# Optimization experiments

Measured on AMD Instinct MI355X. Metric: run time of the kernel, lower is better.

## Reference

```python
import jax, jax.numpy as jnp
import numpy as np

N_NODES = 50000
N_EDGES = 1600000
IN_FEATS = 512
N_HIDDEN = 128
N_CLASSES = 40


def setup_inputs() -> dict:
    key = jax.random.key(0)
    k1, k2, k3, k4, k5, k6, k7 = jax.random.split(key, 7)
    features = jax.random.normal(k1, (N_NODES, IN_FEATS), dtype=jnp.float32)
    src = jax.random.randint(k2, (N_EDGES,), 0, N_NODES)
    dst = jax.random.randint(k3, (N_EDGES,), 0, N_NODES)
    # Glorot-ish init for weights, zeros for biases (DGL GraphConv defaults)
    W1 = jax.random.normal(k4, (IN_FEATS, N_HIDDEN), dtype=jnp.float32) / np.sqrt(IN_FEATS)
    b1 = jnp.zeros((N_HIDDEN,), dtype=jnp.float32)
    W2 = jax.random.normal(k5, (N_HIDDEN, N_CLASSES), dtype=jnp.float32) / np.sqrt(N_HIDDEN)
    b2 = jnp.zeros((N_CLASSES,), dtype=jnp.float32)
    return {"features": features, "W1": W1, "b1": b1, "W2": W2, "b2": b2,
            "src": src, "dst": dst}


def _norms(src, dst, n_nodes):
    ones = jnp.ones(src.shape[0], dtype=jnp.float32)
    deg_out = jax.ops.segment_sum(ones, src, num_segments=n_nodes)
    deg_in = jax.ops.segment_sum(ones, dst, num_segments=n_nodes)
    # clamp degree >= 1 as DGL does
    norm_src = jax.lax.rsqrt(jnp.maximum(deg_out, 1.0))
    norm_dst = jax.lax.rsqrt(jnp.maximum(deg_in, 1.0))
    return norm_src, norm_dst


def _graph_conv(x, W, b, src, dst, norm_src, norm_dst, n_nodes):
    # DGL GraphConv with norm='both'; in_feats > out_feats so W applied first
    h = x @ W                                   # [N, out]
    h = h * norm_src[:, None]                   # src-side D^{-1/2}
    msgs = h[src]                               # gather [E, out]
    agg = jax.ops.segment_sum(msgs, dst, num_segments=n_nodes)  # scatter-add
    agg = agg * norm_dst[:, None]               # dst-side D^{-1/2}
    return agg + b


def reference(features, W1, b1, W2, b2, src, dst):
    norm_src, norm_dst = _norms(src, dst, N_NODES)
    h = _graph_conv(features, W1, b1, src, dst, norm_src, norm_dst, N_NODES)
    h = jax.nn.relu(h)
    # dropout is identity at inference
    h = _graph_conv(h, W2, b2, src, dst, norm_src, norm_dst, N_NODES)
    return h
```

## Files before the change

### kernel.cpp

```cpp
#include <hip/hip_runtime.h>
#include <hip/hip_bf16.h>

#define N_NODES 50000
#define N_EDGES 1600000
#define IN_FEATS 512
#define N_HIDDEN 128
#define N_CLASSES 40
#define NBKT 782
#define NBLK 800
#define EPB 2000
#define NROWPAD 50048

typedef __attribute__((ext_vector_type(8))) short bf16x8;
typedef __attribute__((ext_vector_type(4))) float f32x4;

__device__ __forceinline__ unsigned short f2bf(float f) {
    unsigned u = __float_as_uint(f);
    u = (u + 0x7FFFu + ((u >> 16) & 1u)) >> 16;
    return (unsigned short)u;
}
__device__ __forceinline__ float bf2f(unsigned short h) {
    return __uint_as_float(((unsigned)h) << 16);
}
__device__ __forceinline__ unsigned pk_bf(float a, float b) {
    __hip_bfloat162 h = __float22bfloat162_rn(make_float2(a, b));
    union { __hip_bfloat162 v; unsigned u; } c;
    c.v = h;
    return c.u;
}

__global__ __launch_bounds__(256) void setup_cvt(
    const float* __restrict__ W1, const float* __restrict__ W2,
    unsigned short* __restrict__ W1ch, unsigned short* __restrict__ W1cl,
    unsigned short* __restrict__ W2th, unsigned short* __restrict__ W2tl) {
    int i = blockIdx.x * 256 + threadIdx.x;
    if (i < IN_FEATS * N_HIDDEN) {
        int k = i >> 7, c = i & 127;
        float v = W1[i];
        unsigned short h = f2bf(v);
        int o = (k >> 5) * 4096 + c * 32 + (k & 31);
        W1ch[o] = h;
        W1cl[o] = f2bf(v - bf2f(h));
    } else {
        int j = i - IN_FEATS * N_HIDDEN;
        int n = j >> 7, k = j & 127;
        float v = (n < N_CLASSES) ? W2[k * N_CLASSES + n] : 0.f;
        unsigned short h = f2bf(v);
        W2th[n * 128 + k] = h;
        W2tl[n * 128 + k] = f2bf(v - bf2f(h));
    }
}

__global__ __launch_bounds__(256) void megaA(
    const int* __restrict__ src, const int* __restrict__ dst,
    int* __restrict__ histD, int* __restrict__ histS,
    const float* __restrict__ X, const unsigned short* __restrict__ Wch,
    const unsigned short* __restrict__ Wcl, unsigned short* __restrict__ Hb) {
    __shared__ int hd[NBKT], hs[NBKT];
    __shared__ __align__(16) unsigned short Xh[64][40];
    __shared__ __align__(16) unsigned short Xl[64][40];
    const int tid = threadIdx.x;

    if (blockIdx.x < NBLK) {
        int b = blockIdx.x;
        for (int i = tid; i < NBKT; i += 256) { hd[i] = 0; hs[i] = 0; }
        __syncthreads();
        int e0 = b * EPB;
        for (int i = tid; i < EPB; i += 256) {
            atomicAdd(&hd[dst[e0 + i] >> 6], 1);
            atomicAdd(&hs[src[e0 + i] >> 6], 1);
        }
        __syncthreads();
        for (int i = tid; i < NBKT; i += 256) {
            histD[b * NBKT + i] = hd[i];
            histS[b * NBKT + i] = hs[i];
        }
        return;
    }
    const int lane = tid & 63;
    const int wv = tid >> 6;
    const int m = lane & 15;
    const int q = lane >> 4;
    const int row0 = (blockIdx.x - NBLK) * 64;

    const int r0 = tid >> 3,          kq0 = (tid & 7) * 4;
    const int r1 = (tid + 256) >> 3,  kq1 = (tid & 7) * 4;
    const bool g0 = (row0 + r0) < N_NODES;
    const bool g1 = (row0 + r1) < N_NODES;
    const float* xp0 = &X[(size_t)(row0 + r0) * IN_FEATS + kq0];
    const float* xp1 = &X[(size_t)(row0 + r1) * IN_FEATS + kq1];

    f32x4 acc[4][2];
#pragma unroll
    for (int i = 0; i < 4; i++)
#pragma unroll
        for (int j = 0; j < 2; j++) acc[i][j] = (f32x4){0.f, 0.f, 0.f, 0.f};

    float4 xa0 = g0 ? *(const float4*)xp0 : make_float4(0.f, 0.f, 0.f, 0.f);
    float4 xa1 = g1 ? *(const float4*)xp1 : make_float4(0.f, 0.f, 0.f, 0.f);

    for (int kc = 0; kc < 16; kc++) {
        {
            unsigned h0 = pk_bf(xa0.x, xa0.y), h1 = pk_bf(xa0.z, xa0.w);
            unsigned l0 = pk_bf(xa0.x - __uint_as_float(h0 << 16),
                                xa0.y - __uint_as_float(h0 & 0xffff0000u));
            unsigned l1 = pk_bf(xa0.z - __uint_as_float(h1 << 16),
                                xa0.w - __uint_as_float(h1 & 0xffff0000u));
            *(uint2*)&Xh[r0][kq0] = make_uint2(h0, h1);
            *(uint2*)&Xl[r0][kq0] = make_uint2(l0, l1);
            unsigned h2 = pk_bf(xa1.x, xa1.y), h3 = pk_bf(xa1.z, xa1.w);
            unsigned l2 = pk_bf(xa1.x - __uint_as_float(h2 << 16),
                                xa1.y - __uint_as_float(h2 & 0xffff0000u));
            unsigned l3 = pk_bf(xa1.z - __uint_as_float(h3 << 16),
                                xa1.w - __uint_as_float(h3 & 0xffff0000u));
            *(uint2*)&Xh[r1][kq1] = make_uint2(h2, h3);
            *(uint2*)&Xl[r1][kq1] = make_uint2(l2, l3);
        }
        __syncthreads();
        if (kc < 15) {
            xa0 = g0 ? *(const float4*)(xp0 + (kc + 1) * 32) : make_float4(0.f, 0.f, 0.f, 0.f);
            xa1 = g1 ? *(const float4*)(xp1 + (kc + 1) * 32) : make_float4(0.f, 0.f, 0.f, 0.f);
        }
        bf16x8 bh[2], bl[2];
#pragma unroll
        for (int j = 0; j < 2; j++) {
            int o = kc * 4096 + (wv * 32 + j * 16 + m) * 32 + q * 8;
            bh[j] = *(const bf16x8*)&Wch[o];
            bl[j] = *(const bf16x8*)&Wcl[o];
        }
        bf16x8 ah[4], al[4];
#pragma unroll
        for (int i = 0; i < 4; i++) {
            ah[i] = *(const bf16x8*)&Xh[i * 16 + m][q * 8];
            al[i] = *(const bf16x8*)&Xl[i * 16 + m][q * 8];
        }
#pragma unroll
        for (int i = 0; i < 4; i++)
#pragma unroll
            for (int j = 0; j < 2; j++) {
                acc[i][j] = __builtin_amdgcn_mfma_f32_16x16x32_bf16(ah[i], bh[j], acc[i][j], 0, 0, 0);
                acc[i][j] = __builtin_amdgcn_mfma_f32_16x16x32_bf16(ah[i], bl[j], acc[i][j], 0, 0, 0);
                acc[i][j] = __builtin_amdgcn_mfma_f32_16x16x32_bf16(al[i], bh[j], acc[i][j], 0, 0, 0);
            }
        __syncthreads();
    }
#pragma unroll
    for (int i = 0; i < 4; i++) {
#pragma unroll
        for (int r = 0; r < 4; r++) {
            int grow = row0 + i * 16 + q * 4 + r;
            if (grow < N_NODES) {
#pragma unroll
                for (int j = 0; j < 2; j++)
                    Hb[(size_t)grow * N_HIDDEN + wv * 32 + j * 16 + m] = f2bf(acc[i][j][r]);
            }
        }
    }
}

__global__ __launch_bounds__(256) void p2_local(
    const int* __restrict__ histD, const int* __restrict__ histS,
    int* __restrict__ baseD, int* __restrict__ baseS,
    int* __restrict__ totD, int* __restrict__ totS) {
    int wv = threadIdx.x >> 6, lane = threadIdx.x & 63;
    int w = blockIdx.x * 4 + wv;
    if (w >= NBKT) return;
    int runD = 0, runS = 0;
#pragma unroll
    for (int c = 0; c < 13; c++) {
        int blk = c * 64 + lane;
        int vD = 0, vS = 0;
        if (blk < NBLK) {
            vD = histD[blk * NBKT + w];
            vS = histS[blk * NBKT + w];
        }
        int iD = vD, iS = vS;
#pragma unroll
        for (int off = 1; off < 64; off <<= 1) {
            int tD = __shfl_up(iD, off);
            int tS = __shfl_up(iS, off);
            if (lane >= off) { iD += tD; iS += tS; }
        }
        if (blk < NBLK) {
            baseD[blk * NBKT + w] = runD + iD - vD;
            baseS[blk * NBKT + w] = runS + iS - vS;
        }
        runD += __shfl(iD, 63);
        runS += __shfl(iS, 63);
    }
    if (lane == 0) { totD[w] = runD; totS[w] = runS; }
}

__global__ __launch_bounds__(1024) void p2_small(
    const int* __restrict__ totD, const int* __restrict__ totS,
    int* __restrict__ bucket_base, int* __restrict__ srcb_base,
    int* __restrict__ offsets) {
    __shared__ int part[1024];
    int t = threadIdx.x;
    int v = (t < NBKT) ? totD[t] : 0;
    part[t] = v;
    __syncthreads();
    for (int off = 1; off < 1024; off <<= 1) {
        int x = (t >= off) ? part[t - off] : 0;
        __syncthreads();
        part[t] += x;
        __syncthreads();
    }
    if (t < NBKT) bucket_base[t] = part[t] - v;
    if (t == 0) { bucket_base[NBKT] = N_EDGES; offsets[N_NODES] = N_EDGES; }
    __syncthreads();
    v = (t < NBKT) ? totS[t] : 0;
    part[t] = v;
    __syncthreads();
    for (int off = 1; off < 1024; off <<= 1) {
        int x = (t >= off) ? part[t - off] : 0;
        __syncthreads();
        part[t] += x;
        __syncthreads();
    }
    if (t < NBKT) srcb_base[t] = part[t] - v;
    if (t == 0) srcb_base[NBKT] = N_EDGES;
}

__global__ __launch_bounds__(256) void p3_scatter(
    const int* __restrict__ src, const int* __restrict__ dst,
    const int* __restrict__ baseD, const int* __restrict__ baseS,
    const int* __restrict__ bucket_base, const int* __restrict__ srcb_base,
    unsigned int* __restrict__ edata, unsigned char* __restrict__ srcv) {
    __shared__ int curD[NBKT], curS[NBKT];
    int t = threadIdx.x, b = blockIdx.x;
    for (int i = t; i < NBKT; i += 256) {
        curD[i] = bucket_base[i] + baseD[b * NBKT + i];
        curS[i] = srcb_base[i] + baseS[b * NBKT + i];
    }
    __syncthreads();
    int e0 = b * EPB;
    for (int i = t; i < EPB; i += 256) {
        int s = src[e0 + i], d = dst[e0 + i];
        int slotD = atomicAdd(&curD[d >> 6], 1);
        edata[slotD] = (unsigned)s | ((unsigned)(d & 63) << 16);
        int slotS = atomicAdd(&curS[s >> 6], 1);
        srcv[slotS] = (unsigned char)(s & 63);
    }
}

__global__ __launch_bounds__(256) void p4_fused(
    const int* __restrict__ srcb_base, const unsigned char* __restrict__ srcv,
    const int* __restrict__ bucket_base, const unsigned int* __restrict__ edata,
    int* __restrict__ offsets, float* __restrict__ norm_src,
    float* __restrict__ norm_dst, int* __restrict__ sorted_src) {
    __shared__ int cntS[64], cntD[64], cur[64];
    int t = threadIdx.x, b = blockIdx.x;
    if (t < 64) { cntS[t] = 0; cntD[t] = 0; }
    __syncthreads();
    int s0 = srcb_base[b], s1 = srcb_base[b + 1];
    for (int i = s0 + t; i < s1; i += 256) atomicAdd(&cntS[srcv[i]], 1);
    int d0 = bucket_base[b], d1 = bucket_base[b + 1];
    for (int i = d0 + t; i < d1; i += 256)
        atomicAdd(&cntD[(edata[i] >> 16) & 63], 1);
    __syncthreads();
    if (t == 0) {
        int run = 0;
        for (int i = 0; i < 64; i++) { cur[i] = run; run += cntD[i]; }
    }
    __syncthreads();
    if (t < 64) {
        int node = b * 64 + t;
        if (node < N_NODES) {
            norm_src[node] = rsqrtf(fmaxf((float)cntS[t], 1.0f));
            offsets[node] = d0 + cur[t];
            norm_dst[node] = rsqrtf(fmaxf((float)cntD[t], 1.0f));
        }
    }
    __syncthreads();
    for (int i = d0 + t; i < d1; i += 256) {
        unsigned e = edata[i];
        int slot = atomicAdd(&cur[(e >> 16) & 63], 1);
        sorted_src[d0 + slot] = (int)(e & 0xFFFFu);
    }
}

#define FMA8(W, NS)                                                   \
    acc0 = fmaf(__uint_as_float((W).x << 16), NS, acc0);              \
    acc1 = fmaf(__uint_as_float((W).x & 0xffff0000u), NS, acc1);      \
    acc2 = fmaf(__uint_as_float((W).y << 16), NS, acc2);              \
    acc3 = fmaf(__uint_as_float((W).y & 0xffff0000u), NS, acc3);      \
    acc4 = fmaf(__uint_as_float((W).z << 16), NS, acc4);              \
    acc5 = fmaf(__uint_as_float((W).z & 0xffff0000u), NS, acc5);      \
    acc6 = fmaf(__uint_as_float((W).w << 16), NS, acc6);              \
    acc7 = fmaf(__uint_as_float((W).w & 0xffff0000u), NS, acc7);

__global__ __launch_bounds__(256) void agg1_kernel(
    const int* __restrict__ offsets, const int* __restrict__ sorted_src,
    const unsigned short* __restrict__ Hb, const float* __restrict__ norm_dst,
    const float* __restrict__ norm_src, const float* __restrict__ b1,
    unsigned short* __restrict__ H1h, unsigned short* __restrict__ H1l) {
    int wid = (blockIdx.x * 256 + threadIdx.x) >> 6;
    int lane = threadIdx.x & 63;
    if (wid >= N_NODES) return;
    int start = offsets[wid], end = offsets[wid + 1];
    int quad = lane >> 4;
    int c8 = (lane & 15) * 8;
    float acc0 = 0.f, acc1 = 0.f, acc2 = 0.f, acc3 = 0.f;
    float acc4 = 0.f, acc5 = 0.f, acc6 = 0.f, acc7 = 0.f;
    int base = start;
    for (; base + 16 <= end; base += 16) {
        int e0 = sorted_src[base + quad];
        int e1 = sorted_src[base + 4 + quad];
        int e2 = sorted_src[base + 8 + quad];
        int e3 = sorted_src[base + 12 + quad];
        float n0 = norm_src[e0], n1 = norm_src[e1];
        float n2 = norm_src[e2], n3 = norm_src[e3];
        uint4 w0 = *(const uint4*)&Hb[(size_t)e0 * N_HIDDEN + c8];
        uint4 w1 = *(const uint4*)&Hb[(size_t)e1 * N_HIDDEN + c8];
        uint4 w2 = *(const uint4*)&Hb[(size_t)e2 * N_HIDDEN + c8];
        uint4 w3 = *(const uint4*)&Hb[(size_t)e3 * N_HIDDEN + c8];
        FMA8(w0, n0);
        FMA8(w1, n1);
        FMA8(w2, n2);
        FMA8(w3, n3);
    }
    for (; base + 4 <= end; base += 4) {
        int e = sorted_src[base + quad];
        float n = norm_src[e];
        uint4 w = *(const uint4*)&Hb[(size_t)e * N_HIDDEN + c8];
        FMA8(w, n);
    }
    int rem = end - base;
    if (quad < rem) {
        int e = sorted_src[base + quad];
        float n = norm_src[e];
        uint4 w = *(const uint4*)&Hb[(size_t)e * N_HIDDEN + c8];
        FMA8(w, n);
    }
    acc0 += __shfl_xor(acc0, 16); acc0 += __shfl_xor(acc0, 32);
    acc1 += __shfl_xor(acc1, 16); acc1 += __shfl_xor(acc1, 32);
    acc2 += __shfl_xor(acc2, 16); acc2 += __shfl_xor(acc2, 32);
    acc3 += __shfl_xor(acc3, 16); acc3 += __shfl_xor(acc3, 32);
    acc4 += __shfl_xor(acc4, 16); acc4 += __shfl_xor(acc4, 32);
    acc5 += __shfl_xor(acc5, 16); acc5 += __shfl_xor(acc5, 32);
    acc6 += __shfl_xor(acc6, 16); acc6 += __shfl_xor(acc6, 32);
    acc7 += __shfl_xor(acc7, 16); acc7 += __shfl_xor(acc7, 32);
    if (quad == 0) {
        float nd = norm_dst[wid];
        float ns = norm_src[wid];
        float4 ba = *(const float4*)&b1[c8];
        float4 bb = *(const float4*)&b1[c8 + 4];
        float o[8];
        o[0] = fmaxf(acc0 * nd + ba.x, 0.f) * ns;
        o[1] = fmaxf(acc1 * nd + ba.y, 0.f) * ns;
        o[2] = fmaxf(acc2 * nd + ba.z, 0.f) * ns;
        o[3] = fmaxf(acc3 * nd + ba.w, 0.f) * ns;
        o[4] = fmaxf(acc4 * nd + bb.x, 0.f) * ns;
        o[5] = fmaxf(acc5 * nd + bb.y, 0.f) * ns;
        o[6] = fmaxf(acc6 * nd + bb.z, 0.f) * ns;
        o[7] = fmaxf(acc7 * nd + bb.w, 0.f) * ns;
        unsigned short hh[8], ll[8];
#pragma unroll
        for (int t = 0; t < 8; t++) {
            hh[t] = f2bf(o[t]);
            ll[t] = f2bf(o[t] - bf2f(hh[t]));
        }
        uint4 ph = make_uint4((unsigned)hh[0] | ((unsigned)hh[1] << 16),
                              (unsigned)hh[2] | ((unsigned)hh[3] << 16),
                              (unsigned)hh[4] | ((unsigned)hh[5] << 16),
                              (unsigned)hh[6] | ((unsigned)hh[7] << 16));
        uint4 pl = make_uint4((unsigned)ll[0] | ((unsigned)ll[1] << 16),
                              (unsigned)ll[2] | ((unsigned)ll[3] << 16),
                              (unsigned)ll[4] | ((unsigned)ll[5] << 16),
                              (unsigned)ll[6] | ((unsigned)ll[7] << 16));
        *(uint4*)&H1h[(size_t)wid * N_HIDDEN + c8] = ph;
        *(uint4*)&H1l[(size_t)wid * N_HIDDEN + c8] = pl;
    }
}

__global__ __launch_bounds__(256) void gemm2_kernel(
    const unsigned short* __restrict__ H1h, const unsigned short* __restrict__ H1l,
    const unsigned short* __restrict__ W2th, const unsigned short* __restrict__ W2tl,
    float* __restrict__ H2p) {
    __shared__ __align__(16) unsigned short Bh[48][136];
    __shared__ __align__(16) unsigned short Bl[48][136];
    const int tid = threadIdx.x;
    for (int i = tid; i < 48 * 16; i += 256) {
        int n = i >> 4, kq = (i & 15) * 8;
        *(uint4*)&Bh[n][kq] = *(const uint4*)&W2th[n * 128 + kq];
        *(uint4*)&Bl[n][kq] = *(const uint4*)&W2tl[n * 128 + kq];
    }
    __syncthreads();
    const int lane = tid & 63;
    const int wave = tid >> 6;
    const int m = lane & 15;
    const int q = lane >> 4;
    const int row0 = blockIdx.x * 128 + wave * 32;

    f32x4 acc[2][3];
#pragma unroll
    for (int i = 0; i < 2; i++)
#pragma unroll
        for (int j = 0; j < 3; j++) acc[i][j] = (f32x4){0.f, 0.f, 0.f, 0.f};

#pragma unroll
    for (int kc = 0; kc < 4; kc++) {
        bf16x8 bh[3], bl[3];
#pragma unroll
        for (int j = 0; j < 3; j++) {
            bh[j] = *(const bf16x8*)&Bh[j * 16 + m][kc * 32 + q * 8];
            bl[j] = *(const bf16x8*)&Bl[j * 16 + m][kc * 32 + q * 8];
        }
#pragma unroll
        for (int i = 0; i < 2; i++) {
            size_t ro = (size_t)(row0 + i * 16 + m) * N_HIDDEN + kc * 32 + q * 8;
            bf16x8 ah = *(const bf16x8*)&H1h[ro];
            bf16x8 al = *(const bf16x8*)&H1l[ro];
#pragma unroll
            for (int j = 0; j < 3; j++) {
                acc[i][j] = __builtin_amdgcn_mfma_f32_16x16x32_bf16(ah, bh[j], acc[i][j], 0, 0, 0);
                acc[i][j] = __builtin_amdgcn_mfma_f32_16x16x32_bf16(ah, bl[j], acc[i][j], 0, 0, 0);
                acc[i][j] = __builtin_amdgcn_mfma_f32_16x16x32_bf16(al, bh[j], acc[i][j], 0, 0, 0);
            }
        }
    }
#pragma unroll
    for (int i = 0; i < 2; i++) {
#pragma unroll
        for (int r = 0; r < 4; r++) {
            int row = row0 + i * 16 + q * 4 + r;
            if (row < N_NODES) {
#pragma unroll
                for (int j = 0; j < 3; j++) {
                    int col = j * 16 + m;
                    if (col < N_CLASSES)
                        H2p[(size_t)row * 64 + col] = acc[i][j][r];
                }
            }
        }
    }
}

__global__ __launch_bounds__(256) void agg2_kernel(
    const int* __restrict__ offsets, const int* __restrict__ sorted_src,
    const float* __restrict__ H2p, const float* __restrict__ norm_dst,
    const float* __restrict__ b2, float* __restrict__ OUT) {
    int wid = (blockIdx.x * 256 + threadIdx.x) >> 6;
    int lane = threadIdx.x & 63;
    if (wid >= N_NODES) return;
    int start = offsets[wid], end = offsets[wid + 1];
    int quad = lane >> 4;
    int c4 = (lane & 15) * 4;
    bool active = c4 < N_CLASSES;
    float4 acc = make_float4(0.f, 0.f, 0.f, 0.f);
    int base = start;
    for (; base + 16 <= end; base += 16) {
        int e0 = sorted_src[base + quad];
        int e1 = sorted_src[base + 4 + quad];
        int e2 = sorted_src[base + 8 + quad];
        int e3 = sorted_src[base + 12 + quad];
        if (active) {
            float4 v0 = *(const float4*)&H2p[(size_t)e0 * 64 + c4];
            float4 v1 = *(const float4*)&H2p[(size_t)e1 * 64 + c4];
            float4 v2 = *(const float4*)&H2p[(size_t)e2 * 64 + c4];
            float4 v3 = *(const float4*)&H2p[(size_t)e3 * 64 + c4];
            acc.x += (v0.x + v1.x) + (v2.x + v3.x);
            acc.y += (v0.y + v1.y) + (v2.y + v3.y);
            acc.z += (v0.z + v1.z) + (v2.z + v3.z);
            acc.w += (v0.w + v1.w) + (v2.w + v3.w);
        }
    }
    for (; base + 4 <= end; base += 4) {
        int e = sorted_src[base + quad];
        if (active) {
            float4 v = *(const float4*)&H2p[(size_t)e * 64 + c4];
            acc.x += v.x; acc.y += v.y; acc.z += v.z; acc.w += v.w;
        }
    }
    int rem = end - base;
    if (quad < rem && active) {
        int e = sorted_src[base + quad];
        float4 v = *(const float4*)&H2p[(size_t)e * 64 + c4];
        acc.x += v.x; acc.y += v.y; acc.z += v.z; acc.w += v.w;
    }
    acc.x += __shfl_xor(acc.x, 16); acc.x += __shfl_xor(acc.x, 32);
    acc.y += __shfl_xor(acc.y, 16); acc.y += __shfl_xor(acc.y, 32);
    acc.z += __shfl_xor(acc.z, 16); acc.z += __shfl_xor(acc.z, 32);
    acc.w += __shfl_xor(acc.w, 16); acc.w += __shfl_xor(acc.w, 32);
    if (lane < 10) {
        float nd = norm_dst[wid];
        float4 b = *(const float4*)&b2[lane * 4];
        acc.x = acc.x * nd + b.x;
        acc.y = acc.y * nd + b.y;
        acc.z = acc.z * nd + b.z;
        acc.w = acc.w * nd + b.w;
        *(float4*)&OUT[(size_t)wid * N_CLASSES + lane * 4] = acc;
    }
}

extern "C" void kernel_launch(void* const* d_in, const int* in_sizes, int n_in,
                              void* d_out, int out_size, void* d_ws, size_t ws_size,
                              hipStream_t stream) {
    const float* X   = (const float*)d_in[0];
    const float* W1  = (const float*)d_in[1];
    const float* b1  = (const float*)d_in[2];
    const float* W2  = (const float*)d_in[3];
    const float* b2  = (const float*)d_in[4];
    const int*   src = (const int*)d_in[5];
    const int*   dst = (const int*)d_in[6];
    float* out = (float*)d_out;

    float* norm_src   = (float*)d_ws;
    float* norm_dst   = norm_src + N_NODES;
    int*   offsets    = (int*)(norm_dst + N_NODES);
    int*   bucket_base = offsets + N_NODES + 16;
    int*   srcb_base  = bucket_base + 800;
    unsigned int* edata = (unsigned int*)(srcb_base + 800);
    unsigned char* srcv = (unsigned char*)(edata + N_EDGES);
    int*   sorted_src = (int*)(edata + N_EDGES) + 400000;
    int*   regionA    = sorted_src + N_EDGES;
    int*   histD      = regionA;
    int*   histS      = regionA + 625600;
    int*   baseD      = regionA + 1251200;
    int*   baseS      = regionA + 1876800;
    int*   totD       = regionA + 2502400;
    int*   totS       = regionA + 2503200;
    float* H2p        = (float*)regionA;
    unsigned short* H1h = (unsigned short*)(regionA + 3200000);
    unsigned short* H1l = H1h + (size_t)NROWPAD * N_HIDDEN;
    unsigned short* W1ch = H1l + (size_t)NROWPAD * N_HIDDEN;
    unsigned short* W1cl = W1ch + IN_FEATS * N_HIDDEN;
    unsigned short* W2th = W1cl + IN_FEATS * N_HIDDEN;
    unsigned short* W2tl = W2th + 48 * 128;
    unsigned short* Hb   = W2tl + 48 * 128;

    setup_cvt<<<(IN_FEATS * N_HIDDEN + 48 * 128) / 256, 256, 0, stream>>>(
        W1, W2, W1ch, W1cl, W2th, W2tl);
    megaA<<<NBLK + NBKT, 256, 0, stream>>>(src, dst, histD, histS, X, W1ch, W1cl, Hb);
    p2_local<<<(NBKT + 3) / 4, 256, 0, stream>>>(histD, histS, baseD, baseS, totD, totS);
    p2_small<<<1, 1024, 0, stream>>>(totD, totS, bucket_base, srcb_base, offsets);
    p3_scatter<<<NBLK, 256, 0, stream>>>(src, dst, baseD, baseS, bucket_base, srcb_base,
                                         edata, srcv);
    p4_fused<<<NBKT, 256, 0, stream>>>(srcb_base, srcv, bucket_base, edata,
                                       offsets, norm_src, norm_dst, sorted_src);
    agg1_kernel<<<(N_NODES + 3) / 4, 256, 0, stream>>>(offsets, sorted_src, Hb, norm_dst,
                                                       norm_src, b1, H1h, H1l);
    gemm2_kernel<<<(N_NODES + 127) / 128, 256, 0, stream>>>(H1h, H1l, W2th, W2tl, H2p);
    agg2_kernel<<<(N_NODES + 3) / 4, 256, 0, stream>>>(offsets, sorted_src, H2p, norm_dst, b2, out);
}
```

Measured before the change: 369.0 us.

## Double-buffer X tiles in megaA GEMM with one barrier per k-step

Double-buffers the LDS X tiles in the first-layer GEMM and fully unrolls the 16 k-steps. Each step converts and stores the next chunk while MFMAs run on the current one, with global loads issued two chunks ahead and a single barrier per step instead of two. Histogram and GEMM shared memory now share one raw buffer, and block order is swapped so GEMM blocks come first. The cost is more registers and a larger code footprint.

```diff
diff --git a/kernel.cpp b/kernel.cpp
--- a/kernel.cpp
+++ b/kernel.cpp
@@ -51,18 +51,71 @@
     }
 }
 
+
+#define MF3(AI, BJ, ACC)                                                         \
+    ACC = __builtin_amdgcn_mfma_f32_16x16x32_bf16(ah##AI, bh0##BJ, ACC, 0, 0, 0); \
+    ACC = __builtin_amdgcn_mfma_f32_16x16x32_bf16(ah##AI, bl0##BJ, ACC, 0, 0, 0); \
+    ACC = __builtin_amdgcn_mfma_f32_16x16x32_bf16(al##AI, bh0##BJ, ACC, 0, 0, 0);
+
+#define CONV_STORE(BUF)                                                     \
+    {                                                                       \
+        unsigned h0 = pk_bf(xa0.x, xa0.y), h1 = pk_bf(xa0.z, xa0.w);        \
+        unsigned l0 = pk_bf(xa0.x - __uint_as_float(h0 << 16),              \
+                            xa0.y - __uint_as_float(h0 & 0xffff0000u));     \
+        unsigned l1 = pk_bf(xa0.z - __uint_as_float(h1 << 16),              \
+                            xa0.w - __uint_as_float(h1 & 0xffff0000u));     \
+        *(uint2*)&Xh[BUF][r0][kq0] = make_uint2(h0, h1);                    \
+        *(uint2*)&Xl[BUF][r0][kq0] = make_uint2(l0, l1);                    \
+        unsigned h2 = pk_bf(xa1.x, xa1.y), h3 = pk_bf(xa1.z, xa1.w);        \
+        unsigned l2 = pk_bf(xa1.x - __uint_as_float(h2 << 16),              \
+                            xa1.y - __uint_as_float(h2 & 0xffff0000u));     \
+        unsigned l3 = pk_bf(xa1.z - __uint_as_float(h3 << 16),              \
+                            xa1.w - __uint_as_float(h3 & 0xffff0000u));     \
+        *(uint2*)&Xh[BUF][r1][kq0] = make_uint2(h2, h3);                    \
+        *(uint2*)&Xl[BUF][r1][kq0] = make_uint2(l2, l3);                    \
+    }
+
+#define STEP(CUR, NXT, KC)                                                  \
+    {                                                                       \
+        bf16x8 bh00 = *(const bf16x8*)(wbh + (KC) * 4096);                  \
+        bf16x8 bh01 = *(const bf16x8*)(wbh + (KC) * 4096 + 512);            \
+        bf16x8 bl00 = *(const bf16x8*)(wbl + (KC) * 4096);                  \
+        bf16x8 bl01 = *(const bf16x8*)(wbl + (KC) * 4096 + 512);            \
+        if ((KC) < 14) {                                                    \
+            xn0 = g0 ? *(const float4*)(xp0 + ((KC) + 2) * 32) : f4z;       \
+            xn1 = g1 ? *(const float4*)(xp1 + ((KC) + 2) * 32) : f4z;       \
+        }                                                                   \
+        bf16x8 ah0 = *(const bf16x8*)&Xh[CUR][m][q8];                       \
+        bf16x8 ah1 = *(const bf16x8*)&Xh[CUR][16 + m][q8];                  \
+        bf16x8 ah2 = *(const bf16x8*)&Xh[CUR][32 + m][q8];                  \
+        bf16x8 ah3 = *(const bf16x8*)&Xh[CUR][48 + m][q8];                  \
+        bf16x8 al0 = *(const bf16x8*)&Xl[CUR][m][q8];                       \
+        bf16x8 al1 = *(const bf16x8*)&Xl[CUR][16 + m][q8];                  \
+        bf16x8 al2 = *(const bf16x8*)&Xl[CUR][32 + m][q8];                  \
+        bf16x8 al3 = *(const bf16x8*)&Xl[CUR][48 + m][q8];                  \
+        if ((KC) < 15) {                                                    \
+            CONV_STORE(NXT);                                                \
+            xa0 = xn0; xa1 = xn1;                                           \
+        }                                                                   \
+        MF3(0, 0, acc[0][0]) MF3(0, 1, acc[0][1])                           \
+        MF3(1, 0, acc[1][0]) MF3(1, 1, acc[1][1])                           \
+        MF3(2, 0, acc[2][0]) MF3(2, 1, acc[2][1])                           \
+        MF3(3, 0, acc[3][0]) MF3(3, 1, acc[3][1])                           \
+        if ((KC) < 15) __syncthreads();                                     \
+    }
+
 __global__ __launch_bounds__(256) void megaA(
     const int* __restrict__ src, const int* __restrict__ dst,
     int* __restrict__ histD, int* __restrict__ histS,
     const float* __restrict__ X, const unsigned short* __restrict__ Wch,
     const unsigned short* __restrict__ Wcl, unsigned short* __restrict__ Hb) {
-    __shared__ int hd[NBKT], hs[NBKT];
-    __shared__ __align__(16) unsigned short Xh[64][40];
-    __shared__ __align__(16) unsigned short Xl[64][40];
+    __shared__ __align__(16) unsigned char smem[20480];
     const int tid = threadIdx.x;
 
-    if (blockIdx.x < NBLK) {
-        int b = blockIdx.x;
+    if (blockIdx.x >= NBKT) {
+        int* hd = (int*)smem;
+        int* hs = hd + NBKT;
+        int b = blockIdx.x - NBKT;
         for (int i = tid; i < NBKT; i += 256) { hd[i] = 0; hs[i] = 0; }
         __syncthreads();
         int e0 = b * EPB;
@@ -77,18 +130,25 @@
         }
         return;
     }
+    typedef unsigned short ush;
+    ush (*Xh)[64][40] = (ush(*)[64][40])smem;
+    ush (*Xl)[64][40] = (ush(*)[64][40])(smem + 10240);
+
     const int lane = tid & 63;
     const int wv = tid >> 6;
     const int m = lane & 15;
     const int q = lane >> 4;
-    const int row0 = (blockIdx.x - NBLK) * 64;
-
-    const int r0 = tid >> 3,          kq0 = (tid & 7) * 4;
-    const int r1 = (tid + 256) >> 3,  kq1 = (tid & 7) * 4;
+    const int q8 = q * 8;
+    const int row0 = blockIdx.x * 64;
+
+    const int r0 = tid >> 3, kq0 = (tid & 7) * 4;
+    const int r1 = r0 + 32;
     const bool g0 = (row0 + r0) < N_NODES;
     const bool g1 = (row0 + r1) < N_NODES;
     const float* xp0 = &X[(size_t)(row0 + r0) * IN_FEATS + kq0];
-    const float* xp1 = &X[(size_t)(row0 + r1) * IN_FEATS + kq1];
+    const float* xp1 = &X[(size_t)(row0 + r1) * IN_FEATS + kq0];
+    const unsigned short* wbh = Wch + (wv * 32 + m) * 32 + q8;
+    const unsigned short* wbl = Wcl + (wv * 32 + m) * 32 + q8;
 
     f32x4 acc[4][2];
 #pragma unroll
@@ -96,54 +156,34 @@
 #pragma unroll
         for (int j = 0; j < 2; j++) acc[i][j] = (f32x4){0.f, 0.f, 0.f, 0.f};
 
-    float4 xa0 = g0 ? *(const float4*)xp0 : make_float4(0.f, 0.f, 0.f, 0.f);
-    float4 xa1 = g1 ? *(const float4*)xp1 : make_float4(0.f, 0.f, 0.f, 0.f);
-
-    for (int kc = 0; kc < 16; kc++) {
-        {
-            unsigned h0 = pk_bf(xa0.x, xa0.y), h1 = pk_bf(xa0.z, xa0.w);
-            unsigned l0 = pk_bf(xa0.x - __uint_as_float(h0 << 16),
-                                xa0.y - __uint_as_float(h0 & 0xffff0000u));
-            unsigned l1 = pk_bf(xa0.z - __uint_as_float(h1 << 16),
-                                xa0.w - __uint_as_float(h1 & 0xffff0000u));
-            *(uint2*)&Xh[r0][kq0] = make_uint2(h0, h1);
-            *(uint2*)&Xl[r0][kq0] = make_uint2(l0, l1);
-            unsigned h2 = pk_bf(xa1.x, xa1.y), h3 = pk_bf(xa1.z, xa1.w);
-            unsigned l2 = pk_bf(xa1.x - __uint_as_float(h2 << 16),
-                                xa1.y - __uint_as_float(h2 & 0xffff0000u));
-            unsigned l3 = pk_bf(xa1.z - __uint_as_float(h3 << 16),
-                                xa1.w - __uint_as_float(h3 & 0xffff0000u));
-            *(uint2*)&Xh[r1][kq1] = make_uint2(h2, h3);
-            *(uint2*)&Xl[r1][kq1] = make_uint2(l2, l3);
-        }
-        __syncthreads();
-        if (kc < 15) {
-            xa0 = g0 ? *(const float4*)(xp0 + (kc + 1) * 32) : make_float4(0.f, 0.f, 0.f, 0.f);
-            xa1 = g1 ? *(const float4*)(xp1 + (kc + 1) * 32) : make_float4(0.f, 0.f, 0.f, 0.f);
-        }
-        bf16x8 bh[2], bl[2];
-#pragma unroll
-        for (int j = 0; j < 2; j++) {
-            int o = kc * 4096 + (wv * 32 + j * 16 + m) * 32 + q * 8;
-            bh[j] = *(const bf16x8*)&Wch[o];
-            bl[j] = *(const bf16x8*)&Wcl[o];
-        }
-        bf16x8 ah[4], al[4];
-#pragma unroll
-        for (int i = 0; i < 4; i++) {
-            ah[i] = *(const bf16x8*)&Xh[i * 16 + m][q * 8];
-            al[i] = *(const bf16x8*)&Xl[i * 16 + m][q * 8];
-        }
-#pragma unroll
-        for (int i = 0; i < 4; i++)
-#pragma unroll
-            for (int j = 0; j < 2; j++) {
-                acc[i][j] = __builtin_amdgcn_mfma_f32_16x16x32_bf16(ah[i], bh[j], acc[i][j], 0, 0, 0);
-                acc[i][j] = __builtin_amdgcn_mfma_f32_16x16x32_bf16(ah[i], bl[j], acc[i][j], 0, 0, 0);
-                acc[i][j] = __builtin_amdgcn_mfma_f32_16x16x32_bf16(al[i], bh[j], acc[i][j], 0, 0, 0);
-            }
-        __syncthreads();
-    }
+    const float4 f4z = make_float4(0.f, 0.f, 0.f, 0.f);
+    float4 xa0 = g0 ? *(const float4*)xp0 : f4z;
+    float4 xa1 = g1 ? *(const float4*)xp1 : f4z;
+    float4 xn0 = f4z, xn1 = f4z;
+    {
+        CONV_STORE(0)
+    }
+    xa0 = g0 ? *(const float4*)(xp0 + 32) : f4z;
+    xa1 = g1 ? *(const float4*)(xp1 + 32) : f4z;
+    __syncthreads();
+
+    STEP(0, 1, 0)
+    STEP(1, 0, 1)
+    STEP(0, 1, 2)
+    STEP(1, 0, 3)
+    STEP(0, 1, 4)
+    STEP(1, 0, 5)
+    STEP(0, 1, 6)
+    STEP(1, 0, 7)
+    STEP(0, 1, 8)
+    STEP(1, 0, 9)
+    STEP(0, 1, 10)
+    STEP(1, 0, 11)
+    STEP(0, 1, 12)
+    STEP(1, 0, 13)
+    STEP(0, 1, 14)
+    STEP(1, 0, 15)
+
 #pragma unroll
     for (int i = 0; i < 4; i++) {
 #pragma unroll
```

New measurement: 367.3 us. Within noise of the previous version (-0.5%).

## Load X directly into MFMA registers, dropping LDS staging and block barriers

Applied to the files above, without the earlier changes.

The first-layer GEMM no longer stages bf16 hi/lo splits of X through shared memory. Each lane now loads its X row fragments straight from global memory in MFMA operand layout, converts them in registers, and prefetches the next K chunk. This removes both __syncthreads per K step and the LDS traffic. The cost is that all four waves re-read and re-convert the same 64 rows, roughly quadrupling X load and split work, with the extra reads hopefully served from cache. Block ordering is also swapped so GEMM blocks come before the histogram blocks.

```diff
diff --git a/kernel.cpp b/kernel.cpp
--- a/kernel.cpp
+++ b/kernel.cpp
@@ -27,6 +27,22 @@
     union { __hip_bfloat162 v; unsigned u; } c;
     c.v = h;
     return c.u;
+}
+
+__device__ __forceinline__ void cvt8(float4 a, float4 b, bf16x8& h, bf16x8& l) {
+    unsigned h0 = pk_bf(a.x, a.y), h1 = pk_bf(a.z, a.w);
+    unsigned h2 = pk_bf(b.x, b.y), h3 = pk_bf(b.z, b.w);
+    unsigned l0 = pk_bf(a.x - __uint_as_float(h0 << 16),
+                        a.y - __uint_as_float(h0 & 0xffff0000u));
+    unsigned l1 = pk_bf(a.z - __uint_as_float(h1 << 16),
+                        a.w - __uint_as_float(h1 & 0xffff0000u));
+    unsigned l2 = pk_bf(b.x - __uint_as_float(h2 << 16),
+                        b.y - __uint_as_float(h2 & 0xffff0000u));
+    unsigned l3 = pk_bf(b.z - __uint_as_float(h3 << 16),
+                        b.w - __uint_as_float(h3 & 0xffff0000u));
+    union U { unsigned u[4]; bf16x8 v; };
+    U H; H.u[0] = h0; H.u[1] = h1; H.u[2] = h2; H.u[3] = h3; h = H.v;
+    U L; L.u[0] = l0; L.u[1] = l1; L.u[2] = l2; L.u[3] = l3; l = L.v;
 }
 
 __global__ __launch_bounds__(256) void setup_cvt(
@@ -51,18 +67,39 @@
     }
 }
 
+
+#define MFJ(AH, AL, BH, BL, ACC)                                              \
+    ACC = __builtin_amdgcn_mfma_f32_16x16x32_bf16(AH, BH, ACC, 0, 0, 0);      \
+    ACC = __builtin_amdgcn_mfma_f32_16x16x32_bf16(AH, BL, ACC, 0, 0, 0);      \
+    ACC = __builtin_amdgcn_mfma_f32_16x16x32_bf16(AL, BH, ACC, 0, 0, 0);
+
+#define LOADB(KC)                                                             \
+    const bf16x8 bh0 = *(const bf16x8*)(wbh + (KC) * 4096);                   \
+    const bf16x8 bh1 = *(const bf16x8*)(wbh + (KC) * 4096 + 512);             \
+    const bf16x8 bl0 = *(const bf16x8*)(wbl + (KC) * 4096);                   \
+    const bf16x8 bl1 = *(const bf16x8*)(wbl + (KC) * 4096 + 512);
+
+#define CORE()                                                                \
+    bf16x8 ah0, al0, ah1, al1, ah2, al2, ah3, al3;                            \
+    cvt8(xa00, xa01, ah0, al0); cvt8(xa10, xa11, ah1, al1);                   \
+    cvt8(xa20, xa21, ah2, al2); cvt8(xa30, xa31, ah3, al3);                   \
+    MFJ(ah0, al0, bh0, bl0, acc[0][0]) MFJ(ah0, al0, bh1, bl1, acc[0][1])     \
+    MFJ(ah1, al1, bh0, bl0, acc[1][0]) MFJ(ah1, al1, bh1, bl1, acc[1][1])     \
+    MFJ(ah2, al2, bh0, bl0, acc[2][0]) MFJ(ah2, al2, bh1, bl1, acc[2][1])     \
+    MFJ(ah3, al3, bh0, bl0, acc[3][0]) MFJ(ah3, al3, bh1, bl1, acc[3][1])
+
+__device__ __forceinline__ int imin(int a, int b) { return a < b ? a : b; }
+
 __global__ __launch_bounds__(256) void megaA(
     const int* __restrict__ src, const int* __restrict__ dst,
     int* __restrict__ histD, int* __restrict__ histS,
     const float* __restrict__ X, const unsigned short* __restrict__ Wch,
     const unsigned short* __restrict__ Wcl, unsigned short* __restrict__ Hb) {
     __shared__ int hd[NBKT], hs[NBKT];
-    __shared__ __align__(16) unsigned short Xh[64][40];
-    __shared__ __align__(16) unsigned short Xl[64][40];
     const int tid = threadIdx.x;
 
-    if (blockIdx.x < NBLK) {
-        int b = blockIdx.x;
+    if (blockIdx.x >= NBKT) {
+        int b = blockIdx.x - NBKT;
         for (int i = tid; i < NBKT; i += 256) { hd[i] = 0; hs[i] = 0; }
         __syncthreads();
         int e0 = b * EPB;
@@ -81,14 +118,16 @@
     const int wv = tid >> 6;
     const int m = lane & 15;
     const int q = lane >> 4;
-    const int row0 = (blockIdx.x - NBLK) * 64;
-
-    const int r0 = tid >> 3,          kq0 = (tid & 7) * 4;
-    const int r1 = (tid + 256) >> 3,  kq1 = (tid & 7) * 4;
-    const bool g0 = (row0 + r0) < N_NODES;
-    const bool g1 = (row0 + r1) < N_NODES;
-    const float* xp0 = &X[(size_t)(row0 + r0) * IN_FEATS + kq0];
-    const float* xp1 = &X[(size_t)(row0 + r1) * IN_FEATS + kq1];
+    const int q8 = q * 8;
+    const int row0 = blockIdx.x * 64;
+
+    const unsigned short* wbh = Wch + (wv * 32 + m) * 32 + q8;
+    const unsigned short* wbl = Wcl + (wv * 32 + m) * 32 + q8;
+
+    const float* xr0 = &X[(size_t)imin(row0 + m,      N_NODES - 1) * IN_FEATS + q8];
+    const float* xr1 = &X[(size_t)imin(row0 + 16 + m, N_NODES - 1) * IN_FEATS + q8];
+    const float* xr2 = &X[(size_t)imin(row0 + 32 + m, N_NODES - 1) * IN_FEATS + q8];
+    const float* xr3 = &X[(size_t)imin(row0 + 48 + m, N_NODES - 1) * IN_FEATS + q8];
 
     f32x4 acc[4][2];
 #pragma unroll
@@ -96,54 +135,27 @@
 #pragma unroll
         for (int j = 0; j < 2; j++) acc[i][j] = (f32x4){0.f, 0.f, 0.f, 0.f};
 
-    float4 xa0 = g0 ? *(const float4*)xp0 : make_float4(0.f, 0.f, 0.f, 0.f);
-    float4 xa1 = g1 ? *(const float4*)xp1 : make_float4(0.f, 0.f, 0.f, 0.f);
-
-    for (int kc = 0; kc < 16; kc++) {
-        {
-            unsigned h0 = pk_bf(xa0.x, xa0.y), h1 = pk_bf(xa0.z, xa0.w);
-            unsigned l0 = pk_bf(xa0.x - __uint_as_float(h0 << 16),
-                                xa0.y - __uint_as_float(h0 & 0xffff0000u));
-            unsigned l1 = pk_bf(xa0.z - __uint_as_float(h1 << 16),
-                                xa0.w - __uint_as_float(h1 & 0xffff0000u));
-            *(uint2*)&Xh[r0][kq0] = make_uint2(h0, h1);
-            *(uint2*)&Xl[r0][kq0] = make_uint2(l0, l1);
-            unsigned h2 = pk_bf(xa1.x, xa1.y), h3 = pk_bf(xa1.z, xa1.w);
-            unsigned l2 = pk_bf(xa1.x - __uint_as_float(h2 << 16),
-                                xa1.y - __uint_as_float(h2 & 0xffff0000u));
-            unsigned l3 = pk_bf(xa1.z - __uint_as_float(h3 << 16),
-                                xa1.w - __uint_as_float(h3 & 0xffff0000u));
-            *(uint2*)&Xh[r1][kq1] = make_uint2(h2, h3);
-            *(uint2*)&Xl[r1][kq1] = make_uint2(l2, l3);
-        }
-        __syncthreads();
-        if (kc < 15) {
-            xa0 = g0 ? *(const float4*)(xp0 + (kc + 1) * 32) : make_float4(0.f, 0.f, 0.f, 0.f);
-            xa1 = g1 ? *(const float4*)(xp1 + (kc + 1) * 32) : make_float4(0.f, 0.f, 0.f, 0.f);
-        }
-        bf16x8 bh[2], bl[2];
-#pragma unroll
-        for (int j = 0; j < 2; j++) {
-            int o = kc * 4096 + (wv * 32 + j * 16 + m) * 32 + q * 8;
-            bh[j] = *(const bf16x8*)&Wch[o];
-            bl[j] = *(const bf16x8*)&Wcl[o];
-        }
-        bf16x8 ah[4], al[4];
-#pragma unroll
-        for (int i = 0; i < 4; i++) {
-            ah[i] = *(const bf16x8*)&Xh[i * 16 + m][q * 8];
-            al[i] = *(const bf16x8*)&Xl[i * 16 + m][q * 8];
-        }
-#pragma unroll
-        for (int i = 0; i < 4; i++)
-#pragma unroll
-            for (int j = 0; j < 2; j++) {
-                acc[i][j] = __builtin_amdgcn_mfma_f32_16x16x32_bf16(ah[i], bh[j], acc[i][j], 0, 0, 0);
-                acc[i][j] = __builtin_amdgcn_mfma_f32_16x16x32_bf16(ah[i], bl[j], acc[i][j], 0, 0, 0);
-                acc[i][j] = __builtin_amdgcn_mfma_f32_16x16x32_bf16(al[i], bh[j], acc[i][j], 0, 0, 0);
-            }
-        __syncthreads();
-    }
+    float4 xa00 = *(const float4*)(xr0),     xa01 = *(const float4*)(xr0 + 4);
+    float4 xa10 = *(const float4*)(xr1),     xa11 = *(const float4*)(xr1 + 4);
+    float4 xa20 = *(const float4*)(xr2),     xa21 = *(const float4*)(xr2 + 4);
+    float4 xa30 = *(const float4*)(xr3),     xa31 = *(const float4*)(xr3 + 4);
+
+    for (int kc = 0; kc < 15; kc++) {
+        LOADB(kc)
+        const int o = (kc + 1) * 32;
+        float4 xn00 = *(const float4*)(xr0 + o), xn01 = *(const float4*)(xr0 + o + 4);
+        float4 xn10 = *(const float4*)(xr1 + o), xn11 = *(const float4*)(xr1 + o + 4);
+        float4 xn20 = *(const float4*)(xr2 + o), xn21 = *(const float4*)(xr2 + o + 4);
+        float4 xn30 = *(const float4*)(xr3 + o), xn31 = *(const float4*)(xr3 + o + 4);
+        CORE()
+        xa00 = xn00; xa01 = xn01; xa10 = xn10; xa11 = xn11;
+        xa20 = xn20; xa21 = xn21; xa30 = xn30; xa31 = xn31;
+    }
+    {
+        LOADB(15)
+        CORE()
+    }
+
 #pragma unroll
     for (int i = 0; i < 4; i++) {
 #pragma unroll
```

Result: slower. 389.3 us (+5.5%).
